# Performance work log

Hardware: AMD Instinct MI355X
Metric: run time of the kernel (lower is better)

The kernel has to match this reference:

```python
import jax, jax.numpy as jnp
import numpy as np

DN = ('NCHW', 'OIHW', 'NCHW')

def _conv(x, w, b):
    y = jax.lax.conv_general_dilated(x, w, (2, 2), 'SAME', dimension_numbers=DN)
    return jax.nn.relu(y + b[None, :, None, None])

def setup_inputs() -> dict:
    key = jax.random.key(0)
    ks = jax.random.split(key, 20)
    B, S, V, D, NC = 64, 128, 32000, 512, 1000
    inp = {}
    inp['images'] = jax.random.normal(ks[0], (B, 3, 224, 224), jnp.float32)
    inp['sequences'] = jax.random.randint(ks[1], (B, S), 0, V)
    inp['lengths'] = jax.random.randint(ks[2], (B,), 1, S + 1)
    inp['lengths_var'] = inp['lengths']
    s = 0.02
    inp['emb'] = jax.random.normal(ks[3], (V, D), jnp.float32) * s
    # SimpleCNN(3): 4 strided conv blocks 3->64->128->256->512, final_dim=512
    chans = [3, 64, 128, 256, 512]
    for i in range(4):
        inp[f'cw{i+1}'] = jax.random.normal(ks[4 + i], (chans[i + 1], chans[i], 3, 3), jnp.float32) * s
        inp[f'cb{i+1}'] = jnp.zeros((chans[i + 1],), jnp.float32)
    inp['rnn_w'] = jax.random.normal(ks[8], (D, D), jnp.float32) * s
    inp['rnn_b'] = jnp.zeros((D,), jnp.float32)
    inp['fc1_w'] = jax.random.normal(ks[9], (D + 512, 512), jnp.float32) * s
    inp['fc1_b'] = jnp.zeros((512,), jnp.float32)
    inp['fc2_w'] = jax.random.normal(ks[10], (512, 512), jnp.float32) * s
    inp['fc2_b'] = jnp.zeros((512,), jnp.float32)
    inp['clf_w'] = jax.random.normal(ks[11], (512, NC), jnp.float32) * s
    inp['clf_b'] = jnp.zeros((NC,), jnp.float32)
    return inp

def reference(images, sequences, lengths, lengths_var, emb, cw1, cb1, cw2, cb2, cw3, cb3, cw4, cb4, rnn_w, rnn_b, fc1_w, fc1_b, fc2_w, fc2_b, clf_w, clf_b):
    B, S = sequences.shape
    # masked mean over valid tokens (replaces the per-sample python loop)
    we = emb[sequences]                                   # [B,S,512]
    mask = (jnp.arange(S)[None, :] < lengths[:, None]).astype(we.dtype)
    batch_means = (we * mask[:, :, None]).sum(1) / lengths.astype(we.dtype)[:, None]
    sent = batch_means @ rnn_w + rnn_b                    # [B,512]
    # SimpleCNN + global avg pool -> [B,512,1,1] -> squeeze
    x = _conv(images, cw1, cb1)
    x = _conv(x, cw2, cb2)
    x = _conv(x, cw3, cb3)
    x = _conv(x, cw4, cb4)
    img = x.mean(axis=(2, 3))                             # [B,512]
    feats = jnp.concatenate([img, sent], axis=1)          # [B,1024]
    h = jax.nn.relu(feats @ fc1_w + fc1_b)
    h = jax.nn.relu(h @ fc2_w + fc2_b)                    # dropout = identity (eval)
    return h @ clf_w + clf_b
```

## Files before the change

### kernel.cpp

```cpp
#include <hip/hip_runtime.h>
#include <hip/hip_bf16.h>
#include <cstddef>
#include <cstdint>

typedef unsigned short u16;
typedef __attribute__((ext_vector_type(8))) short bf16x8;
typedef __attribute__((ext_vector_type(4))) float f32x4;
typedef __attribute__((ext_vector_type(8))) unsigned short u16x8;

static __device__ __forceinline__ u16 f2bf(float x) {
  unsigned u = __float_as_uint(x);
  u += 0x7fffu + ((u >> 16) & 1u);
  return (u16)(u >> 16);
}
static __device__ __forceinline__ float bflo(unsigned u) { return __uint_as_float(u << 16); }
static __device__ __forceinline__ float bfhi(unsigned u) { return __uint_as_float(u & 0xffff0000u); }

static __device__ __forceinline__ void gll16(const u16* g, u16* l) {
  __builtin_amdgcn_global_load_lds(
      (const __attribute__((address_space(1))) void*)g,
      (__attribute__((address_space(3))) void*)l, 16, 0, 0);
}

static __device__ __forceinline__ void halo_store(u16* buf, int H, int W, int C,
                                                  long long i) {
  const int c8n = C >> 3;
  const int c8 = (int)(i % c8n);
  long long rem = i / c8n;
  const int p = (int)(rem % (W + 1 + H));
  const int n = (int)(rem / (W + 1 + H));
  int y, x;
  if (p <= W) { y = H; x = p; } else { y = p - (W + 1); x = W; }
  const u16x8 z = {0, 0, 0, 0, 0, 0, 0, 0};
  *(u16x8*)(buf + (((size_t)n * (H + 1) + y) * (W + 1) + x) * C + c8 * 8) = z;
}
__global__ __launch_bounds__(256) void zero_halo3(u16* __restrict__ A,
                                                  u16* __restrict__ B,
                                                  u16* __restrict__ Cb, int nimg) {
  long long i = (long long)blockIdx.x * 256 + threadIdx.x;
  const long long cA = (long long)nimg * 225 * 8;
  const long long cB = (long long)nimg * 113 * 16;
  const long long cC = (long long)nimg * 57 * 32;
  if (i < cA) { halo_store(A, 112, 112, 64, i); return; }
  i -= cA;
  if (i < cB) { halo_store(B, 56, 56, 128, i); return; }
  i -= cB;
  if (i < cC) halo_store(Cb, 28, 28, 256, i);
}

__global__ __launch_bounds__(256) void conv1_s2(
    const float* __restrict__ in,
    const float* __restrict__ w,
    const float* __restrict__ bias,
    u16* __restrict__ out) {
  __shared__ float sw[64 * 27];
  __shared__ float sb[64];
  __shared__ u16 so[256 * 64];
  const int tid = threadIdx.x;
  if (tid < 64) sb[tid] = bias[tid];
  for (int i = tid; i < 64 * 27; i += 256) sw[i] = w[i];
  __syncthreads();
  const int n = blockIdx.y;
  const int by = blockIdx.x / 7, bx = blockIdx.x % 7;
  const int oy = by * 16 + (tid >> 4), ox = bx * 16 + (tid & 15);
  const float* ibase = in + (size_t)n * 3 * 224 * 224 + (size_t)(2 * oy) * 224 + 2 * ox;
  float v[27];
  #pragma unroll
  for (int c = 0; c < 3; ++c)
    #pragma unroll
    for (int r = 0; r < 3; ++r)
      #pragma unroll
      for (int s = 0; s < 3; ++s) {
        const int iy = 2 * oy + r, ix = 2 * ox + s;
        float x = 0.f;
        if (iy < 224 && ix < 224) x = ibase[(size_t)c * 224 * 224 + r * 224 + s];
        v[c * 9 + r * 3 + s] = x;
      }
  #pragma unroll
  for (int kc = 0; kc < 8; ++kc) {
    u16x8 pack;
    #pragma unroll
    for (int k8 = 0; k8 < 8; ++k8) {
      const int k = kc * 8 + k8;
      float a = sb[k];
      const float* wk = &sw[k * 27];
      #pragma unroll
      for (int t = 0; t < 27; ++t) a = fmaf(v[t], wk[t], a);
      pack[k8] = f2bf(fmaxf(a, 0.f));
    }
    *(u16x8*)&so[(tid * 8 + (kc ^ (tid & 7))) * 8] = pack;
  }
  __syncthreads();
  u16* obase = out + (((size_t)n * 113 + by * 16) * 113 + bx * 16) * 64;
  #pragma unroll
  for (int it = 0; it < 8; ++it) {
    const int row = it * 2 + (tid >> 7);
    const int q = tid & 127;
    const int px = q >> 3, c8 = q & 7;
    const int p = row * 16 + px;
    u16x8 v8 = *(const u16x8*)&so[(p * 8 + (c8 ^ (p & 7))) * 8];
    *(u16x8*)(obase + ((size_t)row * 113 + px) * 64 + c8 * 8) = v8;
  }
}

static __device__ __forceinline__ void pack_one(const float* __restrict__ w,
                                                u16* __restrict__ pw,
                                                int CB, int NB, int C, int idx) {
  const int j = idx & 7;
  const int L = (idx >> 3) & 63;
  int t = idx >> 9;
  const int nbg = t % NB; t /= NB;
  const int cb = t % CB;
  const int tap = t / CB;
  const int n = nbg * 16 + (L & 15);
  const int c = cb * 32 + ((L >> 4) << 3) + j;
  pw[idx] = f2bf(w[((size_t)n * C + c) * 9 + tap]);
}
__global__ __launch_bounds__(256) void pack_all(
    const float* __restrict__ w2, const float* __restrict__ w3,
    const float* __restrict__ w4, u16* __restrict__ p2,
    u16* __restrict__ p3, u16* __restrict__ p4) {
  int i = blockIdx.x * 256 + threadIdx.x;
  if (i < 9 * 64 * 128) { pack_one(w2, p2, 2, 8, 64, i); return; }
  i -= 9 * 64 * 128;
  if (i < 9 * 128 * 256) { pack_one(w3, p3, 4, 16, 128, i); return; }
  i -= 9 * 128 * 256;
  if (i < 9 * 256 * 512) pack_one(w4, p4, 8, 32, 256, i);
}

template<int C, int K, int OH, int OW>
__global__ __launch_bounds__(256, 2) void conv3x3s2_mfma(
    const u16* __restrict__ in,
    const u16* __restrict__ pw,
    const float* __restrict__ bias,
    u16* __restrict__ out,
    int M_total) {
  constexpr int IH = 2 * OH, IW = 2 * OW;
  constexpr int PIW = IW + 1;
  constexpr int P = OH * OW;
  constexpr int CB = C / 32, NB = K / 16;
  constexpr int NPH = 9 * CB / 2;
  static_assert((9 * CB) % 2 == 0, "BK=64 needs even step count");

  __shared__ u16 lds[2][16384];

  const int bm = blockIdx.x;
  const int nbh = blockIdx.y;
  const int lane = threadIdx.x & 63, wv = threadIdx.x >> 6;
  const int mh = wv >> 1, nh = wv & 1;

  int s_aoff[4];
  #pragma unroll
  for (int mf = 0; mf < 4; ++mf) {
    int pm = bm * 128 + mh * 64 + mf * 16 + (lane & 15);
    if (pm >= M_total) pm = M_total - 1;
    const int n = pm / P;
    const int p = pm - n * P;
    const int oy = p / OW, ox = p - oy * OW;
    s_aoff[mf] = ((n * (IH + 1) + 2 * oy) * PIW + 2 * ox) * C + ((lane >> 4) << 3);
  }

  f32x4 acc[4][4];
  #pragma unroll
  for (int mf = 0; mf < 4; ++mf)
    #pragma unroll
    for (int nf = 0; nf < 4; ++nf) acc[mf][nf] = (f32x4){0.f, 0.f, 0.f, 0.f};

  auto STAGE = [&](int ph, int buf) {
    const int st0 = 2 * ph;
    const int tap = st0 / CB;
    const int cb0 = st0 & (CB - 1);
    const int r = tap / 3, s = tap - 3 * r;
    u16* Lb = &lds[buf][0];
    if (nh == 0) {
      const int toff = (r * PIW + s) * C + cb0 * 32;
      #pragma unroll
      for (int kk = 0; kk < 2; ++kk)
        #pragma unroll
        for (int mf = 0; mf < 4; ++mf)
          gll16(in + s_aoff[mf] + toff + kk * 32,
                &Lb[(kk * 8 + mh * 4 + mf) * 512]);
    } else {
      const u16* bp = pw + ((size_t)(st0 + mh) * NB + nbh * 8) * 512 + lane * 8;
      #pragma unroll
      for (int nf = 0; nf < 8; ++nf)
        gll16(bp + nf * 512, &Lb[8192 + (mh * 8 + nf) * 512]);
    }
  };
  auto COMPUTE = [&](int buf) {
    u16* Lb = &lds[buf][0];
    bf16x8 a[4][2], b[4][2];
    #pragma unroll
    for (int kk = 0; kk < 2; ++kk) {
      #pragma unroll
      for (int mf = 0; mf < 4; ++mf)
        a[mf][kk] = *(const bf16x8*)&Lb[(kk * 8 + mh * 4 + mf) * 512 + lane * 8];
      #pragma unroll
      for (int nf = 0; nf < 4; ++nf)
        b[nf][kk] = *(const bf16x8*)&Lb[8192 + (kk * 8 + nh * 4 + nf) * 512 + lane * 8];
    }
    #pragma unroll
    for (int kk = 0; kk < 2; ++kk)
      #pragma unroll
      for (int mf = 0; mf < 4; ++mf)
        #pragma unroll
        for (int nf = 0; nf < 4; ++nf)
          acc[mf][nf] = __builtin_amdgcn_mfma_f32_16x16x32_bf16(
              a[mf][kk], b[nf][kk], acc[mf][nf], 0, 0, 0);
  };

  STAGE(0, 0);
  asm volatile("s_waitcnt vmcnt(0)" ::: "memory");
  __builtin_amdgcn_s_barrier();
  __builtin_amdgcn_sched_barrier(0);

  for (int ph = 0; ph < NPH; ++ph) {
    const int buf = ph & 1;
    if (ph + 1 < NPH) STAGE(ph + 1, buf ^ 1);
    __builtin_amdgcn_s_setprio(1);
    COMPUTE(buf);
    __builtin_amdgcn_s_setprio(0);
    asm volatile("s_waitcnt vmcnt(0)" ::: "memory");
    __builtin_amdgcn_s_barrier();
    __builtin_amdgcn_sched_barrier(0);
  }

  const int rowg = (lane >> 4) << 2;
  #pragma unroll
  for (int mf = 0; mf < 4; ++mf)
    #pragma unroll
    for (int nf = 0; nf < 4; ++nf) {
      const int ch = (nbh * 8 + nh * 4 + nf) * 16 + (lane & 15);
      const float bv = bias[ch];
      #pragma unroll
      for (int rr = 0; rr < 4; ++rr) {
        const int pm = bm * 128 + mh * 64 + mf * 16 + rowg + rr;
        if (pm < M_total) {
          const int n = pm / P;
          const int p = pm - n * P;
          const int oy = p / OW, ox = p - oy * OW;
          out[(((size_t)n * (OH + 1) + oy) * (OW + 1) + ox) * K + ch] =
              f2bf(fmaxf(acc[mf][nf][rr] + bv, 0.f));
        }
      }
    }
}

__global__ __launch_bounds__(256) void avgpool_nhwc(
    const u16* __restrict__ in, float* __restrict__ feats, int n0) {
  const int n = blockIdx.x, t = threadIdx.x;
  const u16* p = in + (size_t)n * (15 * 15 * 512) + t * 2;
  float s0 = 0.f, s1 = 0.f;
  for (int y = 0; y < 14; ++y)
    #pragma unroll
    for (int x = 0; x < 14; ++x) {
      unsigned u = *(const unsigned*)(p + (size_t)(y * 15 + x) * 512);
      s0 += bflo(u);
      s1 += bfhi(u);
    }
  float* f = feats + (size_t)(n0 + n) * 1024;
  f[2 * t] = s0 * (1.f / 196.f);
  f[2 * t + 1] = s1 * (1.f / 196.f);
}

__global__ __launch_bounds__(256) void embed_mean_kernel(
    const int* __restrict__ seq, const int* __restrict__ len,
    const float* __restrict__ emb, float* __restrict__ means) {
  __shared__ float part[3][512];
  const int b = blockIdx.x;
  const int L = len[b];
  const int sg = threadIdx.x >> 6;
  const int d0 = (threadIdx.x & 63) * 8;
  float a[8] = {0.f, 0.f, 0.f, 0.f, 0.f, 0.f, 0.f, 0.f};
  for (int s = sg; s < L; s += 4) {
    const float* e = emb + (size_t)seq[b * 128 + s] * 512 + d0;
    float4 v0 = *(const float4*)e, v1 = *(const float4*)(e + 4);
    a[0] += v0.x; a[1] += v0.y; a[2] += v0.z; a[3] += v0.w;
    a[4] += v1.x; a[5] += v1.y; a[6] += v1.z; a[7] += v1.w;
  }
  if (sg) {
    #pragma unroll
    for (int j = 0; j < 8; ++j) part[sg - 1][d0 + j] = a[j];
  }
  __syncthreads();
  if (sg == 0) {
    const float inv = 1.f / (float)L;
    #pragma unroll
    for (int j = 0; j < 8; ++j)
      means[(size_t)b * 512 + d0 + j] =
          (a[j] + part[0][d0 + j] + part[1][d0 + j] + part[2][d0 + j]) * inv;
  }
}

template<int K, int N, bool RELU>
__global__ __launch_bounds__(256) void fc_kernel(
    const float* __restrict__ x, int ldx,
    const float* __restrict__ w, const float* __restrict__ bias,
    float* __restrict__ out, int ldo) {
  __shared__ float row[4][K];
  const int m0 = blockIdx.y * 4;
  for (int i = threadIdx.x; i < 4 * K; i += 256)
    row[i / K][i % K] = x[(size_t)(m0 + i / K) * ldx + (i % K)];
  __syncthreads();
  const int col = blockIdx.x * 256 + threadIdx.x;
  if (col < N) {
    float acc[4][2] = {{0.f, 0.f}, {0.f, 0.f}, {0.f, 0.f}, {0.f, 0.f}};
    for (int k = 0; k < K; k += 2) {
      float w0 = w[(size_t)(k + 0) * N + col];
      float w1 = w[(size_t)(k + 1) * N + col];
      #pragma unroll
      for (int m = 0; m < 4; ++m) {
        acc[m][0] = fmaf(row[m][k + 0], w0, acc[m][0]);
        acc[m][1] = fmaf(row[m][k + 1], w1, acc[m][1]);
      }
    }
    const float bv = bias[col];
    #pragma unroll
    for (int m = 0; m < 4; ++m) {
      float a = acc[m][0] + acc[m][1] + bv;
      out[(size_t)(m0 + m) * ldo + col] = RELU ? fmaxf(a, 0.f) : a;
    }
  }
}

extern "C" void kernel_launch(void* const* d_in, const int* in_sizes, int n_in,
                              void* d_out, int out_size, void* d_ws, size_t ws_size,
                              hipStream_t stream) {
  const float* images = (const float*)d_in[0];
  const int*   seq    = (const int*)d_in[1];
  const int*   len    = (const int*)d_in[2];
  const float* emb    = (const float*)d_in[4];
  const float* cw1 = (const float*)d_in[5];  const float* cb1 = (const float*)d_in[6];
  const float* cw2 = (const float*)d_in[7];  const float* cb2 = (const float*)d_in[8];
  const float* cw3 = (const float*)d_in[9];  const float* cb3 = (const float*)d_in[10];
  const float* cw4 = (const float*)d_in[11]; const float* cb4 = (const float*)d_in[12];
  const float* rnn_w = (const float*)d_in[13]; const float* rnn_b = (const float*)d_in[14];
  const float* fc1_w = (const float*)d_in[15]; const float* fc1_b = (const float*)d_in[16];
  const float* fc2_w = (const float*)d_in[17]; const float* fc2_b = (const float*)d_in[18];
  const float* clf_w = (const float*)d_in[19]; const float* clf_b = (const float*)d_in[20];
  float* out = (float*)d_out;

  const size_t A_E = (size_t)113 * 113 * 64;
  const size_t B_E = (size_t)57 * 57 * 128;
  const size_t C_E = (size_t)29 * 29 * 256;
  const size_t D_E = (size_t)15 * 15 * 512;
  const size_t PW2_E = 9 * 64 * 128, PW3_E = 9 * 128 * 256, PW4_E = 9 * 256 * 512;
  const size_t PER_IMG = (A_E + B_E + C_E + D_E) * 2;
  const size_t FIXED = (PW2_E + PW3_E + PW4_E) * 2 +
                       (size_t)(64 * 512 + 64 * 1024 + 64 * 512 + 64 * 512) * 4;
  int chunk = 64;
  if (ws_size < FIXED + 64 * PER_IMG) {
    size_t avail = (ws_size > FIXED) ? (ws_size - FIXED) : 0;
    size_t c = avail / PER_IMG;
    chunk = (c < 1) ? 1 : (c > 64 ? 64 : (int)c);
  }
  u16* bufA = (u16*)d_ws;
  u16* bufB = bufA + (size_t)chunk * A_E;
  u16* bufC = bufB + (size_t)chunk * B_E;
  u16* bufD = bufC + (size_t)chunk * C_E;
  u16* pw2 = bufD + (size_t)chunk * D_E;
  u16* pw3 = pw2 + PW2_E;
  u16* pw4 = pw3 + PW3_E;
  float* means = (float*)(pw4 + PW4_E);
  float* feats = means + 64 * 512;
  float* h1 = feats + 64 * 1024;
  float* h2 = h1 + 64 * 512;

  {
    const int pk_total = 9 * 64 * 128 + 9 * 128 * 256 + 9 * 256 * 512;
    pack_all<<<(pk_total + 255) / 256, 256, 0, stream>>>(cw2, cw3, cw4, pw2, pw3, pw4);
    long long zt = (long long)chunk * (225 * 8 + 113 * 16 + 57 * 32);
    zero_halo3<<<(int)((zt + 255) / 256), 256, 0, stream>>>(bufA, bufB, bufC, chunk);
  }

  embed_mean_kernel<<<64, 256, 0, stream>>>(seq, len, emb, means);
  fc_kernel<512, 512, false><<<dim3(2, 16), 256, 0, stream>>>(
      means, 512, rnn_w, rnn_b, feats + 512, 1024);

  for (int n0 = 0; n0 < 64; n0 += chunk) {
    int nb = 64 - n0; if (nb > chunk) nb = chunk;
    conv1_s2<<<dim3(49, nb), 256, 0, stream>>>(
        images + (size_t)n0 * 3 * 224 * 224, cw1, cb1, bufA);
    const int M2 = nb * 56 * 56, M3 = nb * 28 * 28, M4 = nb * 14 * 14;
    conv3x3s2_mfma<64, 128, 56, 56><<<dim3((M2 + 127) / 128, 1), 256, 0, stream>>>(
        bufA, pw2, cb2, bufB, M2);
    conv3x3s2_mfma<128, 256, 28, 28><<<dim3((M3 + 127) / 128, 2), 256, 0, stream>>>(
        bufB, pw3, cb3, bufC, M3);
    conv3x3s2_mfma<256, 512, 14, 14><<<dim3((M4 + 127) / 128, 4), 256, 0, stream>>>(
        bufC, pw4, cb4, bufD, M4);
    avgpool_nhwc<<<nb, 256, 0, stream>>>(bufD, feats, n0);
  }

  fc_kernel<1024, 512, true ><<<dim3(2, 16), 256, 0, stream>>>(feats, 1024, fc1_w, fc1_b, h1, 512);
  fc_kernel<512,  512, true ><<<dim3(2, 16), 256, 0, stream>>>(h1,    512,  fc2_w, fc2_b, h2, 512);
  fc_kernel<512, 1000, false><<<dim3(4, 16), 256, 0, stream>>>(h2,    512,  clf_w, clf_b, out, 1000);
}
```

Before: 466.7 us.

## Switch MFMA conv to 512-thread blocks with triple-buffered BK=32 pipeline

```diff
diff --git a/kernel.cpp b/kernel.cpp
--- a/kernel.cpp
+++ b/kernel.cpp
@@ -129,7 +129,7 @@
 }
 
 template<int C, int K, int OH, int OW>
-__global__ __launch_bounds__(256, 2) void conv3x3s2_mfma(
+__global__ __launch_bounds__(512, 6) void conv3x3s2_mfma(
     const u16* __restrict__ in,
     const u16* __restrict__ pw,
     const float* __restrict__ bias,
@@ -139,20 +139,21 @@
   constexpr int PIW = IW + 1;
   constexpr int P = OH * OW;
   constexpr int CB = C / 32, NB = K / 16;
-  constexpr int NPH = 9 * CB / 2;
-  static_assert((9 * CB) % 2 == 0, "BK=64 needs even step count");
-
-  __shared__ u16 lds[2][16384];
+  constexpr int STEPS = 9 * CB;
+  static_assert(STEPS % 3 == 0, "triple-buffer rotation needs STEPS%3==0");
+
+  __shared__ u16 lds[3][8192];
 
   const int bm = blockIdx.x;
   const int nbh = blockIdx.y;
   const int lane = threadIdx.x & 63, wv = threadIdx.x >> 6;
-  const int mh = wv >> 1, nh = wv & 1;
-
-  int s_aoff[4];
-  #pragma unroll
-  for (int mf = 0; mf < 4; ++mf) {
-    int pm = bm * 128 + mh * 64 + mf * 16 + (lane & 15);
+  const int mh = wv >> 1;
+  const int nh = wv & 1;
+
+  int s_aoff[2];
+  #pragma unroll
+  for (int mf = 0; mf < 2; ++mf) {
+    int pm = bm * 128 + mh * 32 + mf * 16 + (lane & 15);
     if (pm >= M_total) pm = M_total - 1;
     const int n = pm / P;
     const int p = pm - n * P;
@@ -160,81 +161,76 @@
     s_aoff[mf] = ((n * (IH + 1) + 2 * oy) * PIW + 2 * ox) * C + ((lane >> 4) << 3);
   }
 
-  f32x4 acc[4][4];
-  #pragma unroll
-  for (int mf = 0; mf < 4; ++mf)
+  f32x4 acc[2][4];
+  #pragma unroll
+  for (int mf = 0; mf < 2; ++mf)
     #pragma unroll
     for (int nf = 0; nf < 4; ++nf) acc[mf][nf] = (f32x4){0.f, 0.f, 0.f, 0.f};
 
-  auto STAGE = [&](int ph, int buf) {
-    const int st0 = 2 * ph;
-    const int tap = st0 / CB;
-    const int cb0 = st0 & (CB - 1);
-    const int r = tap / 3, s = tap - 3 * r;
-    u16* Lb = &lds[buf][0];
+  auto STAGE = [&](int st, int buf) {
     if (nh == 0) {
-      const int toff = (r * PIW + s) * C + cb0 * 32;
-      #pragma unroll
-      for (int kk = 0; kk < 2; ++kk)
-        #pragma unroll
-        for (int mf = 0; mf < 4; ++mf)
-          gll16(in + s_aoff[mf] + toff + kk * 32,
-                &Lb[(kk * 8 + mh * 4 + mf) * 512]);
+      const int cb = st & (CB - 1);
+      const int tap = st / CB;
+      const int r = tap / 3, s = tap - 3 * r;
+      const int toff = (r * PIW + s) * C + cb * 32;
+      #pragma unroll
+      for (int mf = 0; mf < 2; ++mf)
+        gll16(in + s_aoff[mf] + toff, &lds[buf][(mh * 2 + mf) * 512]);
     } else {
-      const u16* bp = pw + ((size_t)(st0 + mh) * NB + nbh * 8) * 512 + lane * 8;
-      #pragma unroll
-      for (int nf = 0; nf < 8; ++nf)
-        gll16(bp + nf * 512, &Lb[8192 + (mh * 8 + nf) * 512]);
+      const u16* bp = pw + ((size_t)st * NB + nbh * 8 + mh * 2) * 512 + lane * 8;
+      #pragma unroll
+      for (int nf = 0; nf < 2; ++nf)
+        gll16(bp + nf * 512, &lds[buf][4096 + (mh * 2 + nf) * 512]);
     }
   };
   auto COMPUTE = [&](int buf) {
-    u16* Lb = &lds[buf][0];
-    bf16x8 a[4][2], b[4][2];
-    #pragma unroll
-    for (int kk = 0; kk < 2; ++kk) {
-      #pragma unroll
-      for (int mf = 0; mf < 4; ++mf)
-        a[mf][kk] = *(const bf16x8*)&Lb[(kk * 8 + mh * 4 + mf) * 512 + lane * 8];
+    bf16x8 a[2], b[4];
+    #pragma unroll
+    for (int mf = 0; mf < 2; ++mf)
+      a[mf] = *(const bf16x8*)&lds[buf][(mh * 2 + mf) * 512 + lane * 8];
+    #pragma unroll
+    for (int nf = 0; nf < 4; ++nf)
+      b[nf] = *(const bf16x8*)&lds[buf][4096 + (nh * 4 + nf) * 512 + lane * 8];
+    #pragma unroll
+    for (int mf = 0; mf < 2; ++mf)
       #pragma unroll
       for (int nf = 0; nf < 4; ++nf)
-        b[nf][kk] = *(const bf16x8*)&Lb[8192 + (kk * 8 + nh * 4 + nf) * 512 + lane * 8];
-    }
-    #pragma unroll
-    for (int kk = 0; kk < 2; ++kk)
-      #pragma unroll
-      for (int mf = 0; mf < 4; ++mf)
-        #pragma unroll
-        for (int nf = 0; nf < 4; ++nf)
-          acc[mf][nf] = __builtin_amdgcn_mfma_f32_16x16x32_bf16(
-              a[mf][kk], b[nf][kk], acc[mf][nf], 0, 0, 0);
+        acc[mf][nf] = __builtin_amdgcn_mfma_f32_16x16x32_bf16(a[mf], b[nf], acc[mf][nf], 0, 0, 0);
   };
+  auto PHASE = [&](int s, int bufC, int bufS) {
+    const bool more = (s + 2) < STEPS;
+    if (more) STAGE(s + 2, bufS);
+    __builtin_amdgcn_s_setprio(1);
+    COMPUTE(bufC);
+    __builtin_amdgcn_s_setprio(0);
+    if (more) asm volatile("s_waitcnt vmcnt(2)" ::: "memory");
+    else      asm volatile("s_waitcnt vmcnt(0)" ::: "memory");
+    __builtin_amdgcn_s_barrier();
+    __builtin_amdgcn_sched_barrier(0);
+  };
 
   STAGE(0, 0);
-  asm volatile("s_waitcnt vmcnt(0)" ::: "memory");
+  STAGE(1, 1);
+  asm volatile("s_waitcnt vmcnt(2)" ::: "memory");
   __builtin_amdgcn_s_barrier();
   __builtin_amdgcn_sched_barrier(0);
 
-  for (int ph = 0; ph < NPH; ++ph) {
-    const int buf = ph & 1;
-    if (ph + 1 < NPH) STAGE(ph + 1, buf ^ 1);
-    __builtin_amdgcn_s_setprio(1);
-    COMPUTE(buf);
-    __builtin_amdgcn_s_setprio(0);
-    asm volatile("s_waitcnt vmcnt(0)" ::: "memory");
-    __builtin_amdgcn_s_barrier();
-    __builtin_amdgcn_sched_barrier(0);
+  for (int st = 0; st < STEPS; st += 3) {
+    PHASE(st + 0, 0, 2);
+    PHASE(st + 1, 1, 0);
+    PHASE(st + 2, 2, 1);
   }
 
   const int rowg = (lane >> 4) << 2;
   #pragma unroll
-  for (int mf = 0; mf < 4; ++mf)
+  for (int mf = 0; mf < 2; ++mf)
     #pragma unroll
     for (int nf = 0; nf < 4; ++nf) {
       const int ch = (nbh * 8 + nh * 4 + nf) * 16 + (lane & 15);
       const float bv = bias[ch];
       #pragma unroll
       for (int rr = 0; rr < 4; ++rr) {
-        const int pm = bm * 128 + mh * 64 + mf * 16 + rowg + rr;
+        const int pm = bm * 128 + mh * 32 + mf * 16 + rowg + rr;
         if (pm < M_total) {
           const int n = pm / P;
           const int p = pm - n * P;
@@ -382,11 +378,11 @@
     conv1_s2<<<dim3(49, nb), 256, 0, stream>>>(
         images + (size_t)n0 * 3 * 224 * 224, cw1, cb1, bufA);
     const int M2 = nb * 56 * 56, M3 = nb * 28 * 28, M4 = nb * 14 * 14;
-    conv3x3s2_mfma<64, 128, 56, 56><<<dim3((M2 + 127) / 128, 1), 256, 0, stream>>>(
+    conv3x3s2_mfma<64, 128, 56, 56><<<dim3((M2 + 127) / 128, 1), 512, 0, stream>>>(
         bufA, pw2, cb2, bufB, M2);
-    conv3x3s2_mfma<128, 256, 28, 28><<<dim3((M3 + 127) / 128, 2), 256, 0, stream>>>(
+    conv3x3s2_mfma<128, 256, 28, 28><<<dim3((M3 + 127) / 128, 2), 512, 0, stream>>>(
         bufB, pw3, cb3, bufC, M3);
-    conv3x3s2_mfma<256, 512, 14, 14><<<dim3((M4 + 127) / 128, 4), 256, 0, stream>>>(
+    conv3x3s2_mfma<256, 512, 14, 14><<<dim3((M4 + 127) / 128, 4), 512, 0, stream>>>(
         bufC, pw4, cb4, bufD, M4);
     avgpool_nhwc<<<nb, 256, 0, stream>>>(bufD, feats, n0);
   }
```

After: 407.6 us. 12.7% less time.
